# Performance work log

Measured on AMD Instinct MI355X. Metric: run time of the kernel, lower is better.

The kernel has to match this reference:

```python
import jax, jax.numpy as jnp
import numpy as np

PATCHES = 196
HEADS = 12


def build_attention_mask(patches, memory_tokens_list, extension=False):
    """Additive mask: masked entries -inf, allowed entries 0. Shape (1, Sq, Skv)."""
    class_tokens = len(memory_tokens_list) + 1
    input_tokens = patches + class_tokens
    total_tokens = input_tokens + sum(memory_tokens_list)
    mask = np.zeros((1, input_tokens, total_tokens), dtype=np.float32)
    mask[:, :, patches + 1:] = -np.inf
    prev = 0
    for i, mtok in enumerate(memory_tokens_list):
        ct = patches + 1 + i
        ms = input_tokens + prev
        me = ms + mtok
        if extension:
            mask[:, ct:, ct] = 0.0
            mask[:, ct:, ms:me] = 0.0
        else:
            mask[:, ct, ct] = 0.0
            mask[:, ct, ms:me] = 0.0
        prev += mtok
    return mask


def setup_inputs() -> dict:
    key = jax.random.key(0)
    ks = jax.random.split(key, 5)
    B, Sq, D, M = 64, PATCHES + 2, 768, 8  # 1 base class token + 1 memory class token
    std = 0.02
    return {
        "hidden_states": jax.random.normal(ks[0], (B, Sq, D), jnp.float32),
        "memory": jax.random.normal(ks[1], (1, M, D), jnp.float32) * std,
        "Wq": jax.random.normal(ks[2], (D, D), jnp.float32) * std,
        "bq": jnp.zeros((D,), jnp.float32),
        "Wk": jax.random.normal(ks[3], (D, D), jnp.float32) * std,
        "bk": jnp.zeros((D,), jnp.float32),
        "Wv": jax.random.normal(ks[4], (D, D), jnp.float32) * std,
        "bv": jnp.zeros((D,), jnp.float32),
    }


def _split_heads(x, heads):
    B, S, D = x.shape
    return x.reshape(B, S, heads, D // heads)  # bshd


def reference(hidden_states, memory, Wq, bq, Wk, bk, Wv, bv):
    B, Sq, D = hidden_states.shape
    M = memory.shape[1]
    head_dim = D // HEADS
    scale = 1.0 / jnp.sqrt(jnp.asarray(head_dim, hidden_states.dtype))
    # static additive mask (1, Sq, Skv)
    mask = jnp.asarray(build_attention_mask(PATCHES, [M]))

    with_memory = jnp.concatenate(
        [hidden_states, jnp.broadcast_to(memory, (B, M, D))], axis=1)  # (B, Skv, D)

    q = _split_heads(hidden_states @ Wq + bq, HEADS)  # (B,Sq,H,dh)
    k = _split_heads(with_memory @ Wk + bk, HEADS)    # (B,Skv,H,dh)
    v = _split_heads(with_memory @ Wv + bv, HEADS)

    scores = jnp.einsum("bqhd,bkhd->bhqk", q, k) * scale + mask[:, None]  # (B,H,Sq,Skv)
    probs = jax.nn.softmax(scores, axis=-1)  # dropout is identity in eval
    ctx = jnp.einsum("bhqk,bkhd->bqhd", probs, v)
    return ctx.reshape(B, Sq, D)
```

## Files before the change

kernel.cpp:

```cpp
#include <hip/hip_runtime.h>

typedef __attribute__((ext_vector_type(8))) short bf16x8;
typedef __attribute__((ext_vector_type(4))) float f32x4;
typedef __attribute__((ext_vector_type(4))) unsigned int u32x4;

#define NB 64
#define SQ 198
#define SKV 206
#define DM 768
#define NH 12
#define NROWS (NB * SKV)
#define NCOL 2304

static __device__ __forceinline__ unsigned short f2b(float f) {
  union { float f; unsigned u; } v; v.f = f;
  unsigned r = v.u + 0x7FFFu + ((v.u >> 16) & 1u);
  return (unsigned short)(r >> 16);
}

typedef const __attribute__((address_space(1))) unsigned int g_u32;
typedef __attribute__((address_space(3))) unsigned int l_u32;
static __device__ __forceinline__ void gload_lds16(const void* g, void* l) {
  __builtin_amdgcn_global_load_lds((g_u32*)g, (l_u32*)l, 16, 0, 0);
}

__global__ __launch_bounds__(256) void k_conv_x(const float* __restrict__ hid,
                                                const float* __restrict__ mem,
                                                unsigned short* __restrict__ xkv) {
  int idx = (blockIdx.x * 256 + threadIdx.x) * 8;
  int r = idx / DM;
  int c = idx - r * DM;
  int b = r / SKV, s = r - b * SKV;
  const float* src = (s < SQ) ? (hid + (b * SQ + s) * DM + c)
                              : (mem + (s - SQ) * DM + c);
  float4 v0 = ((const float4*)src)[0];
  float4 v1 = ((const float4*)src)[1];
  unsigned w0 = f2b(v0.x) | ((unsigned)f2b(v0.y) << 16);
  unsigned w1 = f2b(v0.z) | ((unsigned)f2b(v0.w) << 16);
  unsigned w2 = f2b(v1.x) | ((unsigned)f2b(v1.y) << 16);
  unsigned w3 = f2b(v1.z) | ((unsigned)f2b(v1.w) << 16);
  u32x4 o = {w0, w1, w2, w3};
  *(u32x4*)(xkv + idx) = o;
}

__global__ __launch_bounds__(256) void k_conv_w(const float* __restrict__ Wq,
                                                const float* __restrict__ Wk,
                                                const float* __restrict__ Wv,
                                                unsigned short* __restrict__ wt) {
  __shared__ float L[64][65];
  int w = blockIdx.z;
  int n0 = blockIdx.x * 64, k0 = blockIdx.y * 64;
  const float* W = (w == 0) ? Wq : (w == 1) ? Wk : Wv;
  int tid = threadIdx.x;
#pragma unroll
  for (int i = 0; i < 16; ++i) {
    int idx = i * 256 + tid;
    int lr = idx >> 6, lc = idx & 63;
    L[lr][lc] = W[(k0 + lr) * DM + n0 + lc];
  }
  __syncthreads();
  unsigned short* dst = wt + w * DM * DM;
#pragma unroll
  for (int o = 0; o < 2; ++o) {
    int gi = o * 256 + tid;
    int rn = gi >> 3, g = gi & 7;
    unsigned wrd[4];
#pragma unroll
    for (int jj = 0; jj < 4; ++jj) {
      float f0 = L[g * 8 + jj * 2 + 0][rn];
      float f1 = L[g * 8 + jj * 2 + 1][rn];
      wrd[jj] = f2b(f0) | ((unsigned)f2b(f1) << 16);
    }
    u32x4 o4 = {wrd[0], wrd[1], wrd[2], wrd[3]};
    *(u32x4*)(dst + (n0 + rn) * DM + k0 + g * 8) = o4;
  }
}

__global__ __launch_bounds__(512, 2) void k_gemm(const unsigned short* __restrict__ xkv,
                                                 const unsigned short* __restrict__ wt,
                                                 const float* __restrict__ bq,
                                                 const float* __restrict__ bk,
                                                 const float* __restrict__ bv,
                                                 unsigned short* __restrict__ cout) {
  __shared__ __align__(16) unsigned char smem[131072];
  int o = blockIdx.x, xcd = o & 7, rest = o >> 3;
  int sid = (xcd < 4 ? xcd * 59 : 236 + (xcd - 4) * 58) + rest;
  int mtile = sid / 9, ntile = sid - mtile * 9;
  int row0 = mtile * 256, col0 = ntile * 256;
  int w = ntile / 3;
  int colw0 = (ntile - w * 3) * 256;
  int tid = threadIdx.x, lane = tid & 63, wid = tid >> 6;
  int wm = wid >> 2, wn = wid & 3;
  int l = lane & 15, gq = lane >> 4;
  const unsigned short* wbase = wt + w * DM * DM;

  const unsigned short* aP0;
  const unsigned short* aP1;
  const unsigned short* bP0;
  const unsigned short* bP1;
  {
    int sr = tid >> 2, pg = tid & 3, sg = pg ^ ((sr >> 1) & 3);
    int ar0 = row0 + sr;       if (ar0 > NROWS - 1) ar0 = NROWS - 1;
    int ar1 = row0 + 128 + sr; if (ar1 > NROWS - 1) ar1 = NROWS - 1;
    aP0 = xkv + ar0 * DM + sg * 8;
    aP1 = xkv + ar1 * DM + sg * 8;
    bP0 = wbase + (colw0 + sr) * DM + sg * 8;
    bP1 = wbase + (colw0 + 128 + sr) * DM + sg * 8;
  }
  int ldsW = wid * 1024;

  f32x4 zero = {0.f, 0.f, 0.f, 0.f};
  f32x4 acc[8][4];
#pragma unroll
  for (int i = 0; i < 8; ++i)
#pragma unroll
    for (int j = 0; j < 4; ++j) acc[i][j] = zero;

#pragma unroll
  for (int p = 0; p < 3; ++p) {
    gload_lds16(aP0 + p * 32, smem + p * 16384 + ldsW);
    gload_lds16(aP1 + p * 32, smem + p * 16384 + 8192 + ldsW);
    gload_lds16(bP0 + p * 32, smem + 65536 + p * 16384 + ldsW);
    gload_lds16(bP1 + p * 32, smem + 65536 + p * 16384 + 8192 + ldsW);
  }
  asm volatile("s_waitcnt vmcnt(8)" ::: "memory");
  __builtin_amdgcn_s_barrier();

  int swx = (gq * 16) ^ (((l >> 1) & 3) << 4);
  int aRd = (wm * 128 + l) * 64 + swx;
  int bRd = (wn * 64 + l) * 64 + swx;

#pragma unroll 1
  for (int t = 0; t < 24; ++t) {
    int boA = (t & 3) * 16384;
    int boB = 65536 + boA;
    int io = ((t + 3) & 3) * 16384;
    int kI = (t + 3) * 32;
    bool st = (t < 21);
    bf16x8 af[4], bfr[4];
#pragma unroll
    for (int mi = 0; mi < 4; ++mi) af[mi] = *(const bf16x8*)(smem + boA + aRd + mi * 1024);
#pragma unroll
    for (int ni = 0; ni < 4; ++ni) bfr[ni] = *(const bf16x8*)(smem + boB + bRd + ni * 1024);
    if (st) {
      gload_lds16(aP0 + kI, smem + io + ldsW);
      gload_lds16(aP1 + kI, smem + io + 8192 + ldsW);
    }
    __builtin_amdgcn_s_barrier();
    asm volatile("s_waitcnt lgkmcnt(0)" ::: "memory");
    __builtin_amdgcn_sched_barrier(0);
    __builtin_amdgcn_s_setprio(1);
#pragma unroll
    for (int mi = 0; mi < 4; ++mi)
#pragma unroll
      for (int ni = 0; ni < 4; ++ni)
        acc[mi][ni] = __builtin_amdgcn_mfma_f32_16x16x32_bf16(af[mi], bfr[ni], acc[mi][ni], 0, 0, 0);
    __builtin_amdgcn_s_setprio(0);
    __builtin_amdgcn_s_barrier();
    bf16x8 ag[4];
#pragma unroll
    for (int mi = 0; mi < 4; ++mi) ag[mi] = *(const bf16x8*)(smem + boA + aRd + (4 + mi) * 1024);
    if (st) {
      gload_lds16(bP0 + kI, smem + 65536 + io + ldsW);
      gload_lds16(bP1 + kI, smem + 65536 + io + 8192 + ldsW);
    }
    __builtin_amdgcn_s_barrier();
    asm volatile("s_waitcnt lgkmcnt(0)" ::: "memory");
    __builtin_amdgcn_sched_barrier(0);
    __builtin_amdgcn_s_setprio(1);
#pragma unroll
    for (int mi = 0; mi < 4; ++mi)
#pragma unroll
      for (int ni = 0; ni < 4; ++ni)
        acc[4 + mi][ni] = __builtin_amdgcn_mfma_f32_16x16x32_bf16(ag[mi], bfr[ni], acc[4 + mi][ni], 0, 0, 0);
    __builtin_amdgcn_s_setprio(0);
    if (t < 21)       { asm volatile("s_waitcnt vmcnt(8)" ::: "memory"); }
    else if (t == 21) { asm volatile("s_waitcnt vmcnt(4)" ::: "memory"); }
    else if (t == 22) { asm volatile("s_waitcnt vmcnt(0)" ::: "memory"); }
    __builtin_amdgcn_s_barrier();
  }

  const float* bias = (w == 0) ? bq : (w == 1) ? bk : bv;
  float bb[4];
#pragma unroll
  for (int ni = 0; ni < 4; ++ni) bb[ni] = bias[colw0 + wn * 64 + ni * 16 + l];

  __syncthreads();
#pragma unroll
  for (int mi = 0; mi < 8; ++mi)
#pragma unroll
    for (int ni = 0; ni < 4; ++ni)
#pragma unroll
      for (int rr = 0; rr < 4; ++rr) {
        int row = wm * 128 + mi * 16 + gq * 4 + rr;
        int col = wn * 64 + ni * 16 + l;
        *(unsigned short*)(smem + row * 512 + ((col * 2) ^ ((row & 7) << 4))) =
            f2b(acc[mi][ni][rr] + bb[ni]);
      }
  __syncthreads();
#pragma unroll
  for (int it = 0; it < 16; ++it) {
    int gi = it * 512 + tid;
    int row = gi >> 5, gran = gi & 31;
    if (row0 + row < NROWS) {
      u32x4 v = *(const u32x4*)(smem + row * 512 + ((gran * 16) ^ ((row & 7) << 4)));
      *(u32x4*)(cout + (row0 + row) * NCOL + col0 + gran * 8) = v;
    }
  }
}

static __device__ __forceinline__ int vt_off(int row, int col) {
  return row * 416 + ((col * 2) ^ (((row >> 3) & 1) << 4));
}

__global__ __launch_bounds__(256, 3) void k_attn(const unsigned short* __restrict__ cqkv,
                                                 float* __restrict__ out) {
  __shared__ __align__(16) unsigned short Ksh[208 * 64];
  __shared__ __align__(16) unsigned char  VtB[64 * 416];
  int bh = blockIdx.x;
  int b = bh / NH, h = bh - b * NH;
  int tid = threadIdx.x, lane = tid & 63, wid = tid >> 6;
  int g = lane >> 4, l = lane & 15;
  const unsigned short* Cb = cqkv + (b * SKV) * NCOL + h * 64;

  if (tid < 64) *(unsigned*)(VtB + vt_off(tid, 206)) = 0u;
  for (int i = tid; i < 208 * 8; i += 256) {
    int row = i >> 3, gg = i & 7;
    int srow = (row < SKV) ? row : (SKV - 1);
    u32x4 v = *(const u32x4*)(Cb + srow * NCOL + 768 + gg * 8);
    *(u32x4*)((unsigned char*)Ksh + ((row * 128 + gg * 16) ^ ((row & 7) << 4))) = v;
  }
  for (int i = tid; i < 206 * 8; i += 256) {
    int key = i >> 3, gg = i & 7;
    u32x4 v = *(const u32x4*)(Cb + key * NCOL + 1536 + gg * 8);
    union { u32x4 v4; unsigned short e[8]; } u; u.v4 = v;
#pragma unroll
    for (int j = 0; j < 8; ++j)
      *(unsigned short*)(VtB + vt_off(gg * 8 + j, key)) = u.e[j];
  }
  __syncthreads();

  const float scale = 0.125f;
  f32x4 zero4 = {0.f, 0.f, 0.f, 0.f};
  int srcA = ((g & 1) << 5) + l;
  int srcB = srcA + 16;
  bool hiHalf = (g >= 2);

  for (int qt = wid; qt < 13; qt += 4) {
    int qr = qt * 16 + l;
    int qld = qr > 197 ? 197 : qr;
    const unsigned short* qp = Cb + qld * NCOL + g * 8;
    bf16x8 qa0 = *(const bf16x8*)qp;
    bf16x8 qa1 = *(const bf16x8*)(qp + 32);

    f32x4 sc[13];
#pragma unroll
    for (int nt = 0; nt < 13; ++nt) sc[nt] = zero4;
#pragma unroll
    for (int nt = 0; nt < 13; ++nt) {
      int key = nt * 16 + l;
      int rb = key * 128, sw = (key & 7) << 4, kb = g * 16;
      bf16x8 kb0 = *(const bf16x8*)((const unsigned char*)Ksh + rb + (kb ^ sw));
      bf16x8 kb1 = *(const bf16x8*)((const unsigned char*)Ksh + rb + ((kb + 64) ^ sw));
      sc[nt] = __builtin_amdgcn_mfma_f32_16x16x32_bf16(kb0, qa0, sc[nt], 0, 0, 0);
      sc[nt] = __builtin_amdgcn_mfma_f32_16x16x32_bf16(kb1, qa1, sc[nt], 0, 0, 0);
    }

    float mx = -1e30f;
#pragma unroll
    for (int nt = 0; nt < 13; ++nt)
#pragma unroll
      for (int r = 0; r < 4; ++r) {
        int key = nt * 16 + g * 4 + r;
        float s = sc[nt][r] * scale;
        bool ok = (key < 197 || qr == 197) && (key < SKV);
        s = ok ? s : -1e30f;
        sc[nt][r] = s;
        mx = fmaxf(mx, s);
      }
    mx = fmaxf(mx, __shfl_xor(mx, 16));
    mx = fmaxf(mx, __shfl_xor(mx, 32));
    float sum = 0.f;
#pragma unroll
    for (int nt = 0; nt < 13; ++nt)
#pragma unroll
      for (int r = 0; r < 4; ++r) {
        float p = __expf(sc[nt][r] - mx);
        sc[nt][r] = p;
        sum += p;
      }
    sum += __shfl_xor(sum, 16);
    sum += __shfl_xor(sum, 32);
    float inv = 1.0f / sum;

    unsigned pk0[13], pk1[13];
#pragma unroll
    for (int nt = 0; nt < 13; ++nt) {
      asm("v_cvt_pk_bf16_f32 %0, %1, %2" : "=v"(pk0[nt]) : "v"(sc[nt][0]), "v"(sc[nt][1]));
      asm("v_cvt_pk_bf16_f32 %0, %1, %2" : "=v"(pk1[nt]) : "v"(sc[nt][2]), "v"(sc[nt][3]));
    }

    f32x4 ctx[4];
#pragma unroll
    for (int dt = 0; dt < 4; ++dt) ctx[dt] = zero4;
#pragma unroll
    for (int c = 0; c < 7; ++c) {
      union { unsigned w[4]; bf16x8 v; } pa;
      if (c < 6) {
        int n0 = 2 * c, n1 = 2 * c + 1;
        unsigned a0 = (unsigned)__shfl((int)pk0[n0], srcA), b0 = (unsigned)__shfl((int)pk0[n1], srcA);
        unsigned a1 = (unsigned)__shfl((int)pk1[n0], srcA), b1 = (unsigned)__shfl((int)pk1[n1], srcA);
        unsigned a2 = (unsigned)__shfl((int)pk0[n0], srcB), b2 = (unsigned)__shfl((int)pk0[n1], srcB);
        unsigned a3 = (unsigned)__shfl((int)pk1[n0], srcB), b3 = (unsigned)__shfl((int)pk1[n1], srcB);
        pa.w[0] = hiHalf ? b0 : a0;
        pa.w[1] = hiHalf ? b1 : a1;
        pa.w[2] = hiHalf ? b2 : a2;
        pa.w[3] = hiHalf ? b3 : a3;
      } else {
        unsigned a0 = (unsigned)__shfl((int)pk0[12], srcA);
        unsigned a1 = (unsigned)__shfl((int)pk1[12], srcA);
        unsigned a2 = (unsigned)__shfl((int)pk0[12], srcB);
        unsigned a3 = (unsigned)__shfl((int)pk1[12], srcB);
        pa.w[0] = hiHalf ? 0u : a0;
        pa.w[1] = hiHalf ? 0u : a1;
        pa.w[2] = hiHalf ? 0u : a2;
        pa.w[3] = hiHalf ? 0u : a3;
      }
      int colb = c * 32 + g * 8;
      if (c == 6 && hiHalf) colb = 0;
#pragma unroll
      for (int dt = 0; dt < 4; ++dt) {
        bf16x8 vb = *(const bf16x8*)(VtB + vt_off(dt * 16 + l, colb));
        ctx[dt] = __builtin_amdgcn_mfma_f32_16x16x32_bf16(pa.v, vb, ctx[dt], 0, 0, 0);
      }
    }

    float invr[4];
#pragma unroll
    for (int r = 0; r < 4; ++r) invr[r] = __shfl(inv, g * 4 + r);
#pragma unroll
    for (int dt = 0; dt < 4; ++dt)
#pragma unroll
      for (int r = 0; r < 4; ++r) {
        int qo = qt * 16 + g * 4 + r;
        if (qo < SQ)
          out[(b * SQ + qo) * DM + h * 64 + dt * 16 + l] = ctx[dt][r] * invr[r];
      }
  }
}

extern "C" void kernel_launch(void* const* d_in, const int* in_sizes, int n_in,
                              void* d_out, int out_size, void* d_ws, size_t ws_size,
                              hipStream_t stream) {
  const float* hid = (const float*)d_in[0];
  const float* mem = (const float*)d_in[1];
  const float* Wq  = (const float*)d_in[2];
  const float* bq  = (const float*)d_in[3];
  const float* Wk  = (const float*)d_in[4];
  const float* bk  = (const float*)d_in[5];
  const float* Wv  = (const float*)d_in[6];
  const float* bv  = (const float*)d_in[7];
  float* out = (float*)d_out;

  unsigned short* xkv  = (unsigned short*)d_ws;
  unsigned short* wt   = xkv + NROWS * DM;
  unsigned short* cbuf = wt + 3 * DM * DM;

  k_conv_x<<<dim3(NROWS * DM / 8 / 256), 256, 0, stream>>>(hid, mem, xkv);
  k_conv_w<<<dim3(12, 12, 3), 256, 0, stream>>>(Wq, Wk, Wv, wt);
  k_gemm<<<dim3(468), 512, 0, stream>>>(xkv, wt, bq, bk, bv, cbuf);
  k_attn<<<dim3(NB * NH), 256, 0, stream>>>(cbuf, out);
}
```

Baseline: 104.6 us.

## Shrink GEMM tile to 128x256 with 3-stage LDS pipeline and more blocks

The QKV projection GEMM moves from 256x256 tiles with a 4-deep LDS ring and two half-steps per k-iteration to 128x256 tiles with a 3-stage ring and one barrier per k-step. The grid grows from 468 to 927 blocks, remapped across XCDs, and row bounds checks are dropped because 13184 rows divide evenly by 128. The goal is better CU coverage and occupancy from a smaller LDS footprint and fewer barriers. In exchange, each block reuses loaded data less, and launch_bounds(512,4) may cap VGPRs tightly enough to cause register spills.

```diff
diff --git a/kernel.cpp b/kernel.cpp
--- a/kernel.cpp
+++ b/kernel.cpp
@@ -76,17 +76,17 @@
   }
 }
 
-__global__ __launch_bounds__(512, 2) void k_gemm(const unsigned short* __restrict__ xkv,
+__global__ __launch_bounds__(512, 4) void k_gemm(const unsigned short* __restrict__ xkv,
                                                  const unsigned short* __restrict__ wt,
                                                  const float* __restrict__ bq,
                                                  const float* __restrict__ bk,
                                                  const float* __restrict__ bv,
                                                  unsigned short* __restrict__ cout) {
-  __shared__ __align__(16) unsigned char smem[131072];
+  __shared__ __align__(16) unsigned char smem[73728];
   int o = blockIdx.x, xcd = o & 7, rest = o >> 3;
-  int sid = (xcd < 4 ? xcd * 59 : 236 + (xcd - 4) * 58) + rest;
+  int sid = (xcd < 7 ? xcd * 116 : 812) + (xcd < 7 ? 0 : (xcd - 7) * 115) + rest;
   int mtile = sid / 9, ntile = sid - mtile * 9;
-  int row0 = mtile * 256, col0 = ntile * 256;
+  int row0 = mtile * 128, col0 = ntile * 256;
   int w = ntile / 3;
   int colw0 = (ntile - w * 3) * 256;
   int tid = threadIdx.x, lane = tid & 63, wid = tid >> 6;
@@ -94,90 +94,67 @@
   int l = lane & 15, gq = lane >> 4;
   const unsigned short* wbase = wt + w * DM * DM;
 
-  const unsigned short* aP0;
-  const unsigned short* aP1;
+  const unsigned short* aP;
   const unsigned short* bP0;
   const unsigned short* bP1;
   {
     int sr = tid >> 2, pg = tid & 3, sg = pg ^ ((sr >> 1) & 3);
-    int ar0 = row0 + sr;       if (ar0 > NROWS - 1) ar0 = NROWS - 1;
-    int ar1 = row0 + 128 + sr; if (ar1 > NROWS - 1) ar1 = NROWS - 1;
-    aP0 = xkv + ar0 * DM + sg * 8;
-    aP1 = xkv + ar1 * DM + sg * 8;
+    aP  = xkv   + (row0 + sr) * DM + sg * 8;
     bP0 = wbase + (colw0 + sr) * DM + sg * 8;
     bP1 = wbase + (colw0 + 128 + sr) * DM + sg * 8;
   }
   int ldsW = wid * 1024;
 
   f32x4 zero = {0.f, 0.f, 0.f, 0.f};
-  f32x4 acc[8][4];
-#pragma unroll
-  for (int i = 0; i < 8; ++i)
+  f32x4 acc[4][4];
+#pragma unroll
+  for (int i = 0; i < 4; ++i)
 #pragma unroll
     for (int j = 0; j < 4; ++j) acc[i][j] = zero;
 
 #pragma unroll
-  for (int p = 0; p < 3; ++p) {
-    gload_lds16(aP0 + p * 32, smem + p * 16384 + ldsW);
-    gload_lds16(aP1 + p * 32, smem + p * 16384 + 8192 + ldsW);
-    gload_lds16(bP0 + p * 32, smem + 65536 + p * 16384 + ldsW);
-    gload_lds16(bP1 + p * 32, smem + 65536 + p * 16384 + 8192 + ldsW);
-  }
-  asm volatile("s_waitcnt vmcnt(8)" ::: "memory");
+  for (int p = 0; p < 2; ++p) {
+    int bo = p * 24576;
+    gload_lds16(aP  + p * 32, smem + bo + ldsW);
+    gload_lds16(bP0 + p * 32, smem + bo + 8192 + ldsW);
+    gload_lds16(bP1 + p * 32, smem + bo + 16384 + ldsW);
+  }
+  asm volatile("s_waitcnt vmcnt(3)" ::: "memory");
   __builtin_amdgcn_s_barrier();
 
   int swx = (gq * 16) ^ (((l >> 1) & 3) << 4);
-  int aRd = (wm * 128 + l) * 64 + swx;
-  int bRd = (wn * 64 + l) * 64 + swx;
-
+  int aRd = (wm * 64 + l) * 64 + swx;
+  int bRd = 8192 + (wn * 64 + l) * 64 + swx;
+
+  int q = 0;
+  int qn = 2;
 #pragma unroll 1
   for (int t = 0; t < 24; ++t) {
-    int boA = (t & 3) * 16384;
-    int boB = 65536 + boA;
-    int io = ((t + 3) & 3) * 16384;
-    int kI = (t + 3) * 32;
-    bool st = (t < 21);
-    bf16x8 af[4], bfr[4];
-#pragma unroll
-    for (int mi = 0; mi < 4; ++mi) af[mi] = *(const bf16x8*)(smem + boA + aRd + mi * 1024);
-#pragma unroll
-    for (int ni = 0; ni < 4; ++ni) bfr[ni] = *(const bf16x8*)(smem + boB + bRd + ni * 1024);
-    if (st) {
-      gload_lds16(aP0 + kI, smem + io + ldsW);
-      gload_lds16(aP1 + kI, smem + io + 8192 + ldsW);
-    }
-    __builtin_amdgcn_s_barrier();
-    asm volatile("s_waitcnt lgkmcnt(0)" ::: "memory");
-    __builtin_amdgcn_sched_barrier(0);
+    const unsigned char* bp = smem + q * 24576;
+    if (t < 22) {
+      unsigned char* ip = smem + qn * 24576;
+      int kI = (t + 2) * 32;
+      gload_lds16(aP  + kI, ip + ldsW);
+      gload_lds16(bP0 + kI, ip + 8192 + ldsW);
+      gload_lds16(bP1 + kI, ip + 16384 + ldsW);
+    }
+    bf16x8 a[4], b[4];
+#pragma unroll
+    for (int mi = 0; mi < 4; ++mi) a[mi] = *(const bf16x8*)(bp + aRd + mi * 1024);
+#pragma unroll
+    for (int ni = 0; ni < 4; ++ni) b[ni] = *(const bf16x8*)(bp + bRd + ni * 1024);
     __builtin_amdgcn_s_setprio(1);
 #pragma unroll
     for (int mi = 0; mi < 4; ++mi)
 #pragma unroll
       for (int ni = 0; ni < 4; ++ni)
-        acc[mi][ni] = __builtin_amdgcn_mfma_f32_16x16x32_bf16(af[mi], bfr[ni], acc[mi][ni], 0, 0, 0);
+        acc[mi][ni] = __builtin_amdgcn_mfma_f32_16x16x32_bf16(a[mi], b[ni], acc[mi][ni], 0, 0, 0);
     __builtin_amdgcn_s_setprio(0);
-    __builtin_amdgcn_s_barrier();
-    bf16x8 ag[4];
-#pragma unroll
-    for (int mi = 0; mi < 4; ++mi) ag[mi] = *(const bf16x8*)(smem + boA + aRd + (4 + mi) * 1024);
-    if (st) {
-      gload_lds16(bP0 + kI, smem + 65536 + io + ldsW);
-      gload_lds16(bP1 + kI, smem + 65536 + io + 8192 + ldsW);
-    }
-    __builtin_amdgcn_s_barrier();
-    asm volatile("s_waitcnt lgkmcnt(0)" ::: "memory");
-    __builtin_amdgcn_sched_barrier(0);
-    __builtin_amdgcn_s_setprio(1);
-#pragma unroll
-    for (int mi = 0; mi < 4; ++mi)
-#pragma unroll
-      for (int ni = 0; ni < 4; ++ni)
-        acc[4 + mi][ni] = __builtin_amdgcn_mfma_f32_16x16x32_bf16(ag[mi], bfr[ni], acc[4 + mi][ni], 0, 0, 0);
-    __builtin_amdgcn_s_setprio(0);
-    if (t < 21)       { asm volatile("s_waitcnt vmcnt(8)" ::: "memory"); }
-    else if (t == 21) { asm volatile("s_waitcnt vmcnt(4)" ::: "memory"); }
+    if (t < 22)       { asm volatile("s_waitcnt vmcnt(3)" ::: "memory"); }
     else if (t == 22) { asm volatile("s_waitcnt vmcnt(0)" ::: "memory"); }
     __builtin_amdgcn_s_barrier();
+    q = (q == 2) ? 0 : q + 1;
+    qn = (qn == 2) ? 0 : qn + 1;
   }
 
   const float* bias = (w == 0) ? bq : (w == 1) ? bk : bv;
@@ -187,25 +164,23 @@
 
   __syncthreads();
 #pragma unroll
-  for (int mi = 0; mi < 8; ++mi)
+  for (int mi = 0; mi < 4; ++mi)
 #pragma unroll
     for (int ni = 0; ni < 4; ++ni)
 #pragma unroll
       for (int rr = 0; rr < 4; ++rr) {
-        int row = wm * 128 + mi * 16 + gq * 4 + rr;
+        int row = wm * 64 + mi * 16 + gq * 4 + rr;
         int col = wn * 64 + ni * 16 + l;
         *(unsigned short*)(smem + row * 512 + ((col * 2) ^ ((row & 7) << 4))) =
             f2b(acc[mi][ni][rr] + bb[ni]);
       }
   __syncthreads();
 #pragma unroll
-  for (int it = 0; it < 16; ++it) {
+  for (int it = 0; it < 8; ++it) {
     int gi = it * 512 + tid;
     int row = gi >> 5, gran = gi & 31;
-    if (row0 + row < NROWS) {
-      u32x4 v = *(const u32x4*)(smem + row * 512 + ((gran * 16) ^ ((row & 7) << 4)));
-      *(u32x4*)(cout + (row0 + row) * NCOL + col0 + gran * 8) = v;
-    }
+    u32x4 v = *(const u32x4*)(smem + row * 512 + ((gran * 16) ^ ((row & 7) << 4)));
+    *(u32x4*)(cout + (row0 + row) * NCOL + col0 + gran * 8) = v;
   }
 }
 
@@ -368,6 +343,6 @@
 
   k_conv_x<<<dim3(NROWS * DM / 8 / 256), 256, 0, stream>>>(hid, mem, xkv);
   k_conv_w<<<dim3(12, 12, 3), 256, 0, stream>>>(Wq, Wk, Wv, wt);
-  k_gemm<<<dim3(468), 512, 0, stream>>>(xkv, wt, bq, bk, bv, cbuf);
+  k_gemm<<<dim3(927), 512, 0, stream>>>(xkv, wt, bq, bk, bv, cbuf);
   k_attn<<<dim3(NB * NH), 256, 0, stream>>>(cbuf, out);
 }
```

Result: no change. 103.0 us (-1.6%).

## Restructure QKV GEMM mainloop to double-buffered 64-wide K tiles with quadrant phases

Applied to the files above, without the earlier changes.

The projection GEMM mainloop switches from a 4-stage ring of 32-wide K slices to a 2-stage double buffer of 64-wide K slices. The loop runs 12 iterations instead of 24, and each iteration is split into four MFMA quadrant phases. The LDS row stride and XOR swizzle change to match. Global-to-LDS staging is interleaved across the phases, which halves loop and barrier overhead per unit of K. In exchange there is less prefetch depth, more barriers per iteration, and more live fragment registers.

```diff
diff --git a/kernel.cpp b/kernel.cpp
--- a/kernel.cpp
+++ b/kernel.cpp
@@ -94,20 +94,29 @@
   int l = lane & 15, gq = lane >> 4;
   const unsigned short* wbase = wt + w * DM * DM;
 
-  const unsigned short* aP0;
-  const unsigned short* aP1;
-  const unsigned short* bP0;
-  const unsigned short* bP1;
+  const unsigned short* aPtr[2][2];
+  const unsigned short* bPtr[2][2];
   {
-    int sr = tid >> 2, pg = tid & 3, sg = pg ^ ((sr >> 1) & 3);
-    int ar0 = row0 + sr;       if (ar0 > NROWS - 1) ar0 = NROWS - 1;
-    int ar1 = row0 + 128 + sr; if (ar1 > NROWS - 1) ar1 = NROWS - 1;
-    aP0 = xkv + ar0 * DM + sg * 8;
-    aP1 = xkv + ar1 * DM + sg * 8;
-    bP0 = wbase + (colw0 + sr) * DM + sg * 8;
-    bP1 = wbase + (colw0 + 128 + sr) * DM + sg * 8;
+    int srow = tid >> 3;
+    int sg = (tid & 7) ^ (srow & 7);
+#pragma unroll
+    for (int h = 0; h < 2; ++h)
+#pragma unroll
+      for (int j = 0; j < 2; ++j) {
+        int ra = row0 + h * 128 + j * 64 + srow;
+        if (ra > NROWS - 1) ra = NROWS - 1;
+        aPtr[h][j] = xkv + ra * DM + sg * 8;
+        bPtr[h][j] = wbase + (colw0 + h * 128 + j * 64 + srow) * DM + sg * 8;
+      }
   }
   int ldsW = wid * 1024;
+
+#define STAGE_A(t, h)                                                                   \
+  { gload_lds16(aPtr[h][0] + (t) * 64, smem + ((t) & 1) * 32768 + (h) * 16384 + ldsW);  \
+    gload_lds16(aPtr[h][1] + (t) * 64, smem + ((t) & 1) * 32768 + (h) * 16384 + 8192 + ldsW); }
+#define STAGE_B(t, h)                                                                   \
+  { gload_lds16(bPtr[h][0] + (t) * 64, smem + 65536 + ((t) & 1) * 32768 + (h) * 16384 + ldsW); \
+    gload_lds16(bPtr[h][1] + (t) * 64, smem + 65536 + ((t) & 1) * 32768 + (h) * 16384 + 8192 + ldsW); }
 
   f32x4 zero = {0.f, 0.f, 0.f, 0.f};
   f32x4 acc[8][4];
@@ -116,36 +125,32 @@
 #pragma unroll
     for (int j = 0; j < 4; ++j) acc[i][j] = zero;
 
-#pragma unroll
-  for (int p = 0; p < 3; ++p) {
-    gload_lds16(aP0 + p * 32, smem + p * 16384 + ldsW);
-    gload_lds16(aP1 + p * 32, smem + p * 16384 + 8192 + ldsW);
-    gload_lds16(bP0 + p * 32, smem + 65536 + p * 16384 + ldsW);
-    gload_lds16(bP1 + p * 32, smem + 65536 + p * 16384 + 8192 + ldsW);
-  }
-  asm volatile("s_waitcnt vmcnt(8)" ::: "memory");
+  STAGE_A(0, 0); STAGE_A(0, 1); STAGE_B(0, 0); STAGE_B(0, 1);
+  STAGE_A(1, 0); STAGE_B(1, 0); STAGE_B(1, 1);
+  asm volatile("s_waitcnt vmcnt(6)" ::: "memory");
   __builtin_amdgcn_s_barrier();
 
-  int swx = (gq * 16) ^ (((l >> 1) & 3) << 4);
-  int aRd = (wm * 128 + l) * 64 + swx;
-  int bRd = (wn * 64 + l) * 64 + swx;
+  int colsel0 = ((0 * 4 + gq) ^ (l & 7)) << 4;
+  int colsel1 = ((1 * 4 + gq) ^ (l & 7)) << 4;
+  int rowA = (wm * 128 + l) * 128;
+  int rowB = (wn * 64 + l) * 128;
 
 #pragma unroll 1
-  for (int t = 0; t < 24; ++t) {
-    int boA = (t & 3) * 16384;
-    int boB = 65536 + boA;
-    int io = ((t + 3) & 3) * 16384;
-    int kI = (t + 3) * 32;
-    bool st = (t < 21);
-    bf16x8 af[4], bfr[4];
-#pragma unroll
-    for (int mi = 0; mi < 4; ++mi) af[mi] = *(const bf16x8*)(smem + boA + aRd + mi * 1024);
-#pragma unroll
-    for (int ni = 0; ni < 4; ++ni) bfr[ni] = *(const bf16x8*)(smem + boB + bRd + ni * 1024);
-    if (st) {
-      gload_lds16(aP0 + kI, smem + io + ldsW);
-      gload_lds16(aP1 + kI, smem + io + 8192 + ldsW);
-    }
+  for (int t = 0; t < 12; ++t) {
+    const unsigned char* Ab = smem + (t & 1) * 32768;
+    const unsigned char* Bb = smem + 65536 + (t & 1) * 32768;
+    bf16x8 a0[4][2], a1[4][2], b0[2][2], b1[2][2];
+#pragma unroll
+    for (int mi = 0; mi < 4; ++mi) {
+      a0[mi][0] = *(const bf16x8*)(Ab + rowA + mi * 2048 + colsel0);
+      a0[mi][1] = *(const bf16x8*)(Ab + rowA + mi * 2048 + colsel1);
+    }
+#pragma unroll
+    for (int ni = 0; ni < 2; ++ni) {
+      b0[ni][0] = *(const bf16x8*)(Bb + rowB + ni * 2048 + colsel0);
+      b0[ni][1] = *(const bf16x8*)(Bb + rowB + ni * 2048 + colsel1);
+    }
+    if (t < 11) STAGE_A(t + 1, 1);
     __builtin_amdgcn_s_barrier();
     asm volatile("s_waitcnt lgkmcnt(0)" ::: "memory");
     __builtin_amdgcn_sched_barrier(0);
@@ -153,16 +158,16 @@
 #pragma unroll
     for (int mi = 0; mi < 4; ++mi)
 #pragma unroll
-      for (int ni = 0; ni < 4; ++ni)
-        acc[mi][ni] = __builtin_amdgcn_mfma_f32_16x16x32_bf16(af[mi], bfr[ni], acc[mi][ni], 0, 0, 0);
+      for (int ni = 0; ni < 2; ++ni) {
+        acc[mi][ni] = __builtin_amdgcn_mfma_f32_16x16x32_bf16(a0[mi][0], b0[ni][0], acc[mi][ni], 0, 0, 0);
+        acc[mi][ni] = __builtin_amdgcn_mfma_f32_16x16x32_bf16(a0[mi][1], b0[ni][1], acc[mi][ni], 0, 0, 0);
+      }
     __builtin_amdgcn_s_setprio(0);
     __builtin_amdgcn_s_barrier();
-    bf16x8 ag[4];
-#pragma unroll
-    for (int mi = 0; mi < 4; ++mi) ag[mi] = *(const bf16x8*)(smem + boA + aRd + (4 + mi) * 1024);
-    if (st) {
-      gload_lds16(bP0 + kI, smem + 65536 + io + ldsW);
-      gload_lds16(bP1 + kI, smem + 65536 + io + 8192 + ldsW);
+#pragma unroll
+    for (int ni = 0; ni < 2; ++ni) {
+      b1[ni][0] = *(const bf16x8*)(Bb + rowB + (2 + ni) * 2048 + colsel0);
+      b1[ni][1] = *(const bf16x8*)(Bb + rowB + (2 + ni) * 2048 + colsel1);
     }
     __builtin_amdgcn_s_barrier();
     asm volatile("s_waitcnt lgkmcnt(0)" ::: "memory");
@@ -171,14 +176,48 @@
 #pragma unroll
     for (int mi = 0; mi < 4; ++mi)
 #pragma unroll
-      for (int ni = 0; ni < 4; ++ni)
-        acc[4 + mi][ni] = __builtin_amdgcn_mfma_f32_16x16x32_bf16(ag[mi], bfr[ni], acc[4 + mi][ni], 0, 0, 0);
+      for (int ni = 0; ni < 2; ++ni) {
+        acc[mi][2 + ni] = __builtin_amdgcn_mfma_f32_16x16x32_bf16(a0[mi][0], b1[ni][0], acc[mi][2 + ni], 0, 0, 0);
+        acc[mi][2 + ni] = __builtin_amdgcn_mfma_f32_16x16x32_bf16(a0[mi][1], b1[ni][1], acc[mi][2 + ni], 0, 0, 0);
+      }
     __builtin_amdgcn_s_setprio(0);
-    if (t < 21)       { asm volatile("s_waitcnt vmcnt(8)" ::: "memory"); }
-    else if (t == 21) { asm volatile("s_waitcnt vmcnt(4)" ::: "memory"); }
-    else if (t == 22) { asm volatile("s_waitcnt vmcnt(0)" ::: "memory"); }
-    __builtin_amdgcn_s_barrier();
-  }
+    __builtin_amdgcn_s_barrier();
+#pragma unroll
+    for (int mi = 0; mi < 4; ++mi) {
+      a1[mi][0] = *(const bf16x8*)(Ab + rowA + (4 + mi) * 2048 + colsel0);
+      a1[mi][1] = *(const bf16x8*)(Ab + rowA + (4 + mi) * 2048 + colsel1);
+    }
+    if (t < 10) STAGE_B(t + 2, 0);
+    __builtin_amdgcn_s_barrier();
+    asm volatile("s_waitcnt lgkmcnt(0)" ::: "memory");
+    __builtin_amdgcn_sched_barrier(0);
+    __builtin_amdgcn_s_setprio(1);
+#pragma unroll
+    for (int mi = 0; mi < 4; ++mi)
+#pragma unroll
+      for (int ni = 0; ni < 2; ++ni) {
+        acc[4 + mi][ni] = __builtin_amdgcn_mfma_f32_16x16x32_bf16(a1[mi][0], b0[ni][0], acc[4 + mi][ni], 0, 0, 0);
+        acc[4 + mi][ni] = __builtin_amdgcn_mfma_f32_16x16x32_bf16(a1[mi][1], b0[ni][1], acc[4 + mi][ni], 0, 0, 0);
+      }
+    __builtin_amdgcn_s_setprio(0);
+    __builtin_amdgcn_s_barrier();
+    if (t < 10) { STAGE_B(t + 2, 1); STAGE_A(t + 2, 0); }
+    __builtin_amdgcn_s_barrier();
+    __builtin_amdgcn_s_setprio(1);
+#pragma unroll
+    for (int mi = 0; mi < 4; ++mi)
+#pragma unroll
+      for (int ni = 0; ni < 2; ++ni) {
+        acc[4 + mi][2 + ni] = __builtin_amdgcn_mfma_f32_16x16x32_bf16(a1[mi][0], b1[ni][0], acc[4 + mi][2 + ni], 0, 0, 0);
+        acc[4 + mi][2 + ni] = __builtin_amdgcn_mfma_f32_16x16x32_bf16(a1[mi][1], b1[ni][1], acc[4 + mi][2 + ni], 0, 0, 0);
+      }
+    __builtin_amdgcn_s_setprio(0);
+    if (t < 10)       { asm volatile("s_waitcnt vmcnt(6)" ::: "memory"); }
+    else              { asm volatile("s_waitcnt vmcnt(0)" ::: "memory"); }
+    __builtin_amdgcn_s_barrier();
+  }
+#undef STAGE_A
+#undef STAGE_B
 
   const float* bias = (w == 0) ? bq : (w == 1) ? bk : bv;
   float bb[4];
```

Result: no change. 103.3 us (-1.2%).
